# Performance work log

Measured on AMD Instinct MI355X. Metric: run time of the kernel, lower is better.

## Reference

```python
import jax, jax.numpy as jnp
import numpy as np

B, S, D, H = 4, 1024, 1024, 16
HD = D // H  # head_dim = 64


def _xavier(k, shape):
    fan_in, fan_out = shape[1], shape[0]
    limit = float(np.sqrt(6.0 / (fan_in + fan_out)))
    return jax.random.uniform(k, shape, jnp.float32, -limit, limit)


def setup_inputs() -> dict:
    key = jax.random.key(0)
    ks = jax.random.split(key, 12)
    inp = {
        "query": jax.random.normal(ks[0], (B, S, D), jnp.float32),
        "key": jax.random.normal(ks[1], (B, S, D), jnp.float32),
        "value": jax.random.normal(ks[2], (B, S, D), jnp.float32),
        "mask": jax.random.randint(ks[3], (B, 1, 1, S), 0, 2, jnp.int32),
        # Linear weights stored torch-style [out, in]; biases zero-ish (torch default uniform, use zeros-free small init)
        "Wq": _xavier(ks[4], (D, D)), "bq": jnp.zeros((D,), jnp.float32),
        "Wk": _xavier(ks[5], (D, D)), "bk": jnp.zeros((D,), jnp.float32),
        "Wv": _xavier(ks[6], (D, D)), "bv": jnp.zeros((D,), jnp.float32),
        "Wo": _xavier(ks[7], (D, D)), "bo": jnp.zeros((D,), jnp.float32),
    }
    return inp


def reference(query, key, value, mask, Wq, bq, Wk, bk, Wv, bv, Wo, bo):
    # Projections (torch Linear: x @ W.T + b)
    q = query @ Wq.T + bq
    k = key @ Wk.T + bk
    v = value @ Wv.T + bv
    # Split heads -> [B, H, S, HD]
    def split(x):
        b, s, _ = x.shape
        return x.reshape(b, s, H, HD).transpose(0, 2, 1, 3)
    q, k, v = split(q), split(k), split(v)
    scores = jnp.einsum('bhqd,bhkd->bhqk', q, k) / jnp.sqrt(jnp.float32(HD))
    scores = jnp.where(mask == 0, jnp.float32(-1e10), scores)
    attn = jax.nn.softmax(scores, axis=-1)  # dropout is identity in eval
    ctx = jnp.einsum('bhqk,bhkd->bhqd', attn, v)
    ctx = ctx.transpose(0, 2, 1, 3).reshape(ctx.shape[0], -1, D)
    out = ctx @ Wo.T + bo
    return out, attn
```

## Files before the change

### kernel.cpp

```cpp
#include <hip/hip_runtime.h>

constexpr int Bc = 4, Sc = 1024, Dc = 1024, Hc = 16, HDc = 64;
constexpr long BSD = (long)Bc * Sc * Dc;
constexpr long MM  = (long)Dc * Dc;

typedef __attribute__((ext_vector_type(8))) short bf16x8;
typedef __attribute__((ext_vector_type(4))) float f32x4;
typedef unsigned int u32;

__device__ inline ushort f2bf(float f) {
    union { float f; unsigned i; } v; v.f = f;
    unsigned lsb = (v.i >> 16) & 1;
    v.i += 0x7fffu + lsb;
    return (ushort)(v.i >> 16);
}

__global__ __launch_bounds__(256)
void cvt_all(const float* __restrict__ q, const float* __restrict__ k,
             const float* __restrict__ v, const float* __restrict__ Wq,
             const float* __restrict__ Wk, const float* __restrict__ Wv,
             const float* __restrict__ Wo, ushort* __restrict__ dst)
{
    const int t = blockIdx.y;
    const long n = (t < 3) ? BSD : MM;
    const long i = ((long)blockIdx.x * 256 + threadIdx.x) * 8;
    if (i >= n) return;
    const float* src; long off;
    switch (t) {
        case 0: src = q;  off = 0;            break;
        case 1: src = k;  off = BSD;          break;
        case 2: src = v;  off = 2 * BSD;      break;
        case 3: src = Wq; off = 3 * BSD;      break;
        case 4: src = Wk; off = 3 * BSD + MM; break;
        case 5: src = Wv; off = 3 * BSD + 2 * MM; break;
        default: src = Wo; off = 3 * BSD + 3 * MM; break;
    }
    f32x4 a = *(const f32x4*)(src + i);
    f32x4 b = *(const f32x4*)(src + i + 4);
    bf16x8 r;
    #pragma unroll
    for (int j = 0; j < 4; j++) { r[j] = (short)f2bf(a[j]); r[j + 4] = (short)f2bf(b[j]); }
    *(bf16x8*)(dst + off + i) = r;
}

__device__ inline void stage_tile(const ushort* __restrict__ G, int ld, int rowbase,
                                  int kt, ushort* lds, int wave, int lane)
{
    #pragma unroll
    for (int j = 0; j < 2; j++) {
        const int c = wave * 128 + j * 64 + lane;
        const int row = c >> 2, k8 = c & 3;
        const ushort* g = G + (long)(rowbase + row) * ld + kt + k8 * 8;
        ushort* l = lds + (wave * 128 + j * 64) * 8;
        __builtin_amdgcn_global_load_lds(
            (const __attribute__((address_space(1))) u32*)(const void*)g,
            (__attribute__((address_space(3))) u32*)(void*)l, 16, 0, 0);
    }
}

__device__ inline void gemm_core(const ushort* __restrict__ A, int lda,
                                 const ushort* __restrict__ Bt, int ldb, int K,
                                 int mtile, int ntile,
                                 ushort (*As)[128 * 32], ushort (*Bs)[128 * 32],
                                 f32x4 (*acc)[4], int wave, int lane)
{
    const int l15 = lane & 15, quad = lane >> 4;
    const int wr = wave >> 1, wc = wave & 1;

    stage_tile(A,  lda, mtile, 0, As[0], wave, lane);
    stage_tile(Bt, ldb, ntile, 0, Bs[0], wave, lane);
    __syncthreads();

    int buf = 0;
    for (int kt = 0; kt < K; kt += 32) {
        if (kt + 32 < K) {
            stage_tile(A,  lda, mtile, kt + 32, As[buf ^ 1], wave, lane);
            stage_tile(Bt, ldb, ntile, kt + 32, Bs[buf ^ 1], wave, lane);
        }
        bf16x8 af[4], bfr[4];
        #pragma unroll
        for (int mt = 0; mt < 4; mt++)
            af[mt] = *(const bf16x8*)(As[buf] + (wr * 64 + mt * 16 + l15) * 32 + quad * 8);
        #pragma unroll
        for (int nt = 0; nt < 4; nt++)
            bfr[nt] = *(const bf16x8*)(Bs[buf] + (wc * 64 + nt * 16 + l15) * 32 + quad * 8);
        #pragma unroll
        for (int mt = 0; mt < 4; mt++)
            #pragma unroll
            for (int nt = 0; nt < 4; nt++)
                acc[mt][nt] = __builtin_amdgcn_mfma_f32_16x16x32_bf16(af[mt], bfr[nt], acc[mt][nt], 0, 0, 0);
        __syncthreads();
        buf ^= 1;
    }
}

__global__ __launch_bounds__(256)
void gemm_qkv(const ushort* __restrict__ ws, const float* __restrict__ bq,
              const float* __restrict__ bk, const float* __restrict__ bv,
              ushort* __restrict__ QK, ushort* __restrict__ Vt)
{
    __shared__ ushort As[2][128 * 32];
    __shared__ ushort Bs[2][128 * 32];

    const int z = blockIdx.z;
    const ushort* A  = ws + (long)z * BSD;
    const ushort* Bt = ws + 3 * BSD + (long)z * MM;
    const float* bias = (z == 0) ? bq : (z == 1) ? bk : bv;

    const int lane = threadIdx.x & 63, wave = threadIdx.x >> 6;
    const int l15 = lane & 15, quad = lane >> 4;
    const int wr = wave >> 1, wc = wave & 1;
    const int mtile = blockIdx.y * 128, ntile = blockIdx.x * 128;

    f32x4 acc[4][4] = {};
    gemm_core(A, Dc, Bt, Dc, Dc, mtile, ntile, As, Bs, acc, wave, lane);

    #pragma unroll
    for (int mt = 0; mt < 4; mt++) {
        #pragma unroll
        for (int nt = 0; nt < 4; nt++) {
            const int col = ntile + wc * 64 + nt * 16 + l15;
            const float bb = bias[col];
            #pragma unroll
            for (int i = 0; i < 4; i++) {
                const int r = mtile + wr * 64 + mt * 16 + quad * 4 + i;
                const float vv = acc[mt][nt][i] + bb;
                if (z < 2) {
                    QK[(long)z * BSD + (long)r * Dc + col] = f2bf(vv);
                } else {
                    const int b = r >> 10, sI = r & 1023;
                    const int hh = col >> 6, dd = col & 63;
                    Vt[(long)((b * Hc + hh) * HDc + dd) * Sc + sI] = f2bf(vv);
                }
            }
        }
    }
}

__global__ __launch_bounds__(256)
void gemm_out(const ushort* __restrict__ A, const ushort* __restrict__ Bt,
              const float* __restrict__ bias, float* __restrict__ C)
{
    __shared__ ushort As[2][128 * 32];
    __shared__ ushort Bs[2][128 * 32];

    const int lane = threadIdx.x & 63, wave = threadIdx.x >> 6;
    const int l15 = lane & 15, quad = lane >> 4;
    const int wr = wave >> 1, wc = wave & 1;
    const int mtile = blockIdx.y * 128, ntile = blockIdx.x * 128;

    f32x4 acc[4][4] = {};
    gemm_core(A, Dc, Bt, Dc, Dc, mtile, ntile, As, Bs, acc, wave, lane);

    #pragma unroll
    for (int mt = 0; mt < 4; mt++) {
        #pragma unroll
        for (int nt = 0; nt < 4; nt++) {
            const int col = ntile + wc * 64 + nt * 16 + l15;
            const float bb = bias[col];
            #pragma unroll
            for (int i = 0; i < 4; i++) {
                const int r = mtile + wr * 64 + mt * 16 + quad * 4 + i;
                C[(long)r * Dc + col] = acc[mt][nt][i] + bb;
            }
        }
    }
}

__global__ __launch_bounds__(256, 3)
void attn_fused(const ushort* __restrict__ Q, const ushort* __restrict__ Kp,
                const ushort* __restrict__ Vt, const int* __restrict__ mask,
                float* __restrict__ attn, ushort* __restrict__ Ctx)
{
    __shared__ ushort pB[16 * 1024];
    __shared__ float red[2][4][16];

    const int bh = blockIdx.y;
    const int b = bh >> 4, h = bh & 15;
    const int qbase = blockIdx.x * 16;
    const int lane = threadIdx.x & 63;
    const int wave = threadIdx.x >> 6;
    const int l15 = lane & 15, quad = lane >> 4;

    const ushort* Qh = Q  + (long)b * Sc * Dc + h * HDc;
    const ushort* Kh = Kp + (long)b * Sc * Dc + h * HDc;

    const ushort* qrow = Qh + (long)(qbase + l15) * Dc + quad * 8;
    const bf16x8 a0 = *(const bf16x8*)(qrow);
    const bf16x8 a1 = *(const bf16x8*)(qrow + 32);

    f32x4 sacc[16];
    #pragma unroll
    for (int t = 0; t < 16; t++) {
        const int ct = wave * 16 + t;
        const ushort* krow = Kh + (long)(ct * 16 + l15) * Dc + quad * 8;
        const bf16x8 b0 = *(const bf16x8*)(krow);
        const bf16x8 b1 = *(const bf16x8*)(krow + 32);
        f32x4 acc = {};
        acc = __builtin_amdgcn_mfma_f32_16x16x32_bf16(a0, b0, acc, 0, 0, 0);
        acc = __builtin_amdgcn_mfma_f32_16x16x32_bf16(a1, b1, acc, 0, 0, 0);
        sacc[t] = acc;
    }

    unsigned mbits = 0;
    #pragma unroll
    for (int t = 0; t < 16; t++)
        if (mask[b * Sc + (wave * 16 + t) * 16 + l15] == 0) mbits |= (1u << t);

    float mx[4] = { -3.0e38f, -3.0e38f, -3.0e38f, -3.0e38f };
    #pragma unroll
    for (int t = 0; t < 16; t++) {
        const bool msk = (mbits >> t) & 1;
        #pragma unroll
        for (int i = 0; i < 4; i++) {
            float s = sacc[t][i] * 0.125f;
            s = msk ? -1e10f : s;
            sacc[t][i] = s;
            mx[i] = fmaxf(mx[i], s);
        }
    }
    #pragma unroll
    for (int off = 1; off <= 8; off <<= 1)
        #pragma unroll
        for (int i = 0; i < 4; i++) mx[i] = fmaxf(mx[i], __shfl_xor(mx[i], off, 64));
    if (l15 == 0)
        #pragma unroll
        for (int i = 0; i < 4; i++) red[0][wave][quad * 4 + i] = mx[i];
    __syncthreads();
    #pragma unroll
    for (int i = 0; i < 4; i++) {
        float g = red[0][0][quad * 4 + i];
        #pragma unroll
        for (int w = 1; w < 4; w++) g = fmaxf(g, red[0][w][quad * 4 + i]);
        mx[i] = g;
    }

    float sm[4] = { 0.f, 0.f, 0.f, 0.f };
    #pragma unroll
    for (int t = 0; t < 16; t++)
        #pragma unroll
        for (int i = 0; i < 4; i++) {
            const float e = __expf(sacc[t][i] - mx[i]);
            sacc[t][i] = e;
            sm[i] += e;
        }
    #pragma unroll
    for (int off = 1; off <= 8; off <<= 1)
        #pragma unroll
        for (int i = 0; i < 4; i++) sm[i] += __shfl_xor(sm[i], off, 64);
    if (l15 == 0)
        #pragma unroll
        for (int i = 0; i < 4; i++) red[1][wave][quad * 4 + i] = sm[i];
    __syncthreads();
    float inv[4];
    #pragma unroll
    for (int i = 0; i < 4; i++) {
        float g = red[1][0][quad * 4 + i] + red[1][1][quad * 4 + i]
                + red[1][2][quad * 4 + i] + red[1][3][quad * 4 + i];
        inv[i] = 1.0f / g;
    }

    #pragma unroll
    for (int t = 0; t < 16; t++) {
        const int col = (wave * 16 + t) * 16 + l15;
        #pragma unroll
        for (int i = 0; i < 4; i++) {
            const float p = sacc[t][i] * inv[i];
            const int r = quad * 4 + i;
            attn[((long)bh * Sc + qbase + r) * Sc + col] = p;
            const int u = (col >> 2) ^ ((r & 7) << 1);
            pB[r * 1024 + (u << 2) + (col & 3)] = f2bf(p);
        }
    }
    __syncthreads();

    f32x4 pacc[4] = {};
    const ushort* prow = pB + l15 * 1024;
    const int sw2 = (l15 & 7) << 1;
    const ushort* Vh = Vt + (long)bh * HDc * Sc + (long)(wave * 16 + l15) * Sc + quad * 8;
    for (int k0 = 0; k0 < Sc; k0 += 128) {
        bf16x8 af[4], bv4[4];
        #pragma unroll
        for (int u = 0; u < 4; u++) {
            const int k = k0 + u * 32 + quad * 8;
            af[u]  = *(const bf16x8*)(prow + (((k >> 2) ^ sw2) << 2));
            bv4[u] = *(const bf16x8*)(Vh + k0 + u * 32);
        }
        __builtin_amdgcn_s_setprio(1);
        #pragma unroll
        for (int u = 0; u < 4; u++)
            pacc[u] = __builtin_amdgcn_mfma_f32_16x16x32_bf16(af[u], bv4[u], pacc[u], 0, 0, 0);
        __builtin_amdgcn_s_setprio(0);
    }
    f32x4 acc;
    #pragma unroll
    for (int i = 0; i < 4; i++) acc[i] = (pacc[0][i] + pacc[1][i]) + (pacc[2][i] + pacc[3][i]);

    const int dcol = h * HDc + wave * 16 + l15;
    #pragma unroll
    for (int i = 0; i < 4; i++) {
        const int r = qbase + quad * 4 + i;
        Ctx[(long)b * Sc * Dc + (long)r * Dc + dcol] = f2bf(acc[i]);
    }
}

extern "C" void kernel_launch(void* const* d_in, const int* in_sizes, int n_in,
                              void* d_out, int out_size, void* d_ws, size_t ws_size,
                              hipStream_t stream)
{
    const float* q    = (const float*)d_in[0];
    const float* k    = (const float*)d_in[1];
    const float* v    = (const float*)d_in[2];
    const int*   mask = (const int*)  d_in[3];
    const float* Wq   = (const float*)d_in[4];
    const float* bq   = (const float*)d_in[5];
    const float* Wk   = (const float*)d_in[6];
    const float* bk   = (const float*)d_in[7];
    const float* Wv   = (const float*)d_in[8];
    const float* bv   = (const float*)d_in[9];
    const float* Wo   = (const float*)d_in[10];
    const float* bo   = (const float*)d_in[11];

    ushort* ws  = (ushort*)d_ws;
    ushort* Wob = ws + 3 * BSD + 3 * MM;
    ushort* Qp  = ws + 3 * BSD + 4 * MM;
    ushort* Kpp = Qp + BSD;
    ushort* Vt  = Kpp + BSD;
    ushort* Ctx = Vt + BSD;

    float* out  = (float*)d_out;
    float* attn = out + BSD;

    const dim3 blk(256);

    cvt_all<<<dim3(BSD / (256 * 8), 7), blk, 0, stream>>>(q, k, v, Wq, Wk, Wv, Wo, ws);

    gemm_qkv<<<dim3(8, 32, 3), blk, 0, stream>>>(ws, bq, bk, bv, Qp, Vt);

    attn_fused<<<dim3(Sc / 16, Bc * Hc), blk, 0, stream>>>(Qp, Kpp, Vt, mask, attn, Ctx);

    gemm_out<<<dim3(8, 32), blk, 0, stream>>>(Ctx, Wob, bo, out);
}
```

Baseline: 510.3 us.

## Use 128x64 tiles in output GEMM and remap attention blocks per XCD

The output projection GEMM moves from 128x128 to 128x64 tiles with its own K loop, which doubles the grid from 256 to 512 blocks so more of the CUs have work. The attention kernel remaps its linear block index so that each XCD handles eight (batch, head) pairs, keeping that XCD's K/V reads in its own L2. Smaller tiles lower per-block arithmetic intensity and the inlined loop duplicates gemm_core logic.

```diff
diff --git a/kernel.cpp b/kernel.cpp
--- a/kernel.cpp
+++ b/kernel.cpp
@@ -56,6 +56,18 @@
             (const __attribute__((address_space(1))) u32*)(const void*)g,
             (__attribute__((address_space(3))) u32*)(void*)l, 16, 0, 0);
     }
+}
+
+__device__ inline void stage_tile64(const ushort* __restrict__ G, int ld, int rowbase,
+                                    int kt, ushort* lds, int wave, int lane)
+{
+    const int c = wave * 64 + lane;
+    const int row = c >> 2, k8 = c & 3;
+    const ushort* g = G + (long)(rowbase + row) * ld + kt + k8 * 8;
+    ushort* l = lds + wave * 512;
+    __builtin_amdgcn_global_load_lds(
+        (const __attribute__((address_space(1))) u32*)(const void*)g,
+        (__attribute__((address_space(3))) u32*)(void*)l, 16, 0, 0);
 }
 
 __device__ inline void gemm_core(const ushort* __restrict__ A, int lda,
@@ -142,21 +154,46 @@
               const float* __restrict__ bias, float* __restrict__ C)
 {
     __shared__ ushort As[2][128 * 32];
-    __shared__ ushort Bs[2][128 * 32];
+    __shared__ ushort Bs[2][64 * 32];
 
     const int lane = threadIdx.x & 63, wave = threadIdx.x >> 6;
     const int l15 = lane & 15, quad = lane >> 4;
     const int wr = wave >> 1, wc = wave & 1;
-    const int mtile = blockIdx.y * 128, ntile = blockIdx.x * 128;
-
-    f32x4 acc[4][4] = {};
-    gemm_core(A, Dc, Bt, Dc, Dc, mtile, ntile, As, Bs, acc, wave, lane);
+    const int mtile = blockIdx.y * 128, ntile = blockIdx.x * 64;
+
+    f32x4 acc[4][2] = {};
+
+    stage_tile  (A,  Dc, mtile, 0, As[0], wave, lane);
+    stage_tile64(Bt, Dc, ntile, 0, Bs[0], wave, lane);
+    __syncthreads();
+
+    int buf = 0;
+    for (int kt = 0; kt < Dc; kt += 32) {
+        if (kt + 32 < Dc) {
+            stage_tile  (A,  Dc, mtile, kt + 32, As[buf ^ 1], wave, lane);
+            stage_tile64(Bt, Dc, ntile, kt + 32, Bs[buf ^ 1], wave, lane);
+        }
+        bf16x8 af[4], bfr[2];
+        #pragma unroll
+        for (int mt = 0; mt < 4; mt++)
+            af[mt] = *(const bf16x8*)(As[buf] + (wr * 64 + mt * 16 + l15) * 32 + quad * 8);
+        #pragma unroll
+        for (int nt = 0; nt < 2; nt++)
+            bfr[nt] = *(const bf16x8*)(Bs[buf] + (wc * 32 + nt * 16 + l15) * 32 + quad * 8);
+        #pragma unroll
+        for (int mt = 0; mt < 4; mt++)
+            #pragma unroll
+            for (int nt = 0; nt < 2; nt++)
+                acc[mt][nt] = __builtin_amdgcn_mfma_f32_16x16x32_bf16(af[mt], bfr[nt], acc[mt][nt], 0, 0, 0);
+        __syncthreads();
+        buf ^= 1;
+    }
 
     #pragma unroll
     for (int mt = 0; mt < 4; mt++) {
         #pragma unroll
-        for (int nt = 0; nt < 4; nt++) {
-            const int col = ntile + wc * 64 + nt * 16 + l15;
+        for (int nt = 0; nt < 2; nt++) {
+            const int col = ntile + wc * 32 + nt * 16 + l15;
             const float bb = bias[col];
             #pragma unroll
             for (int i = 0; i < 4; i++) {
@@ -175,9 +212,13 @@
     __shared__ ushort pB[16 * 1024];
     __shared__ float red[2][4][16];
 
-    const int bh = blockIdx.y;
+    const int lin  = blockIdx.y * gridDim.x + blockIdx.x;
+    const int xcd  = lin & 7;
+    const int slot = lin >> 3;
+    const int bh    = xcd * 8 + (slot & 7);
+    const int qbase = (slot >> 3) * 16;
+
     const int b = bh >> 4, h = bh & 15;
-    const int qbase = blockIdx.x * 16;
     const int lane = threadIdx.x & 63;
     const int wave = threadIdx.x >> 6;
     const int l15 = lane & 15, quad = lane >> 4;
@@ -339,5 +380,5 @@
 
     attn_fused<<<dim3(Sc / 16, Bc * Hc), blk, 0, stream>>>(Qp, Kpp, Vt, mask, attn, Ctx);
 
-    gemm_out<<<dim3(8, 32), blk, 0, stream>>>(Ctx, Wob, bo, out);
-}
+    gemm_out<<<dim3(16, 32), blk, 0, stream>>>(Ctx, Wob, bo, out);
+}
```

Measured after the change: 512.9 us. Within noise of the previous version (+0.5%).
